# Optimization experiments

Hardware: AMD Instinct MI355X
Metric: run time of the kernel (lower is better)

Reference implementation:

```python
import jax, jax.numpy as jnp
import numpy as np

NUM_USER = 100000
NUM_ENTITY = 1000000
NUM_RELATION = 60
DIM = 32
N_NEIGHBOR = 16
N_ITER = 2
BATCH = 8192


def setup_inputs() -> dict:
    key = jax.random.key(0)
    ks = jax.random.split(key, 9)
    users = jax.random.randint(ks[0], (BATCH,), 0, NUM_USER)
    items = jax.random.randint(ks[1], (BATCH,), 0, NUM_ENTITY)
    entity_emb = jax.random.normal(ks[2], (NUM_ENTITY, DIM), dtype=jnp.float32) * 0.1
    relation_emb = jax.random.normal(ks[3], (NUM_RELATION, DIM), dtype=jnp.float32) * 0.1
    adj_entity = jax.random.randint(ks[4], (NUM_ENTITY, N_NEIGHBOR), 0, NUM_ENTITY)
    adj_relation = jax.random.randint(ks[5], (NUM_ENTITY, N_NEIGHBOR), 0, NUM_RELATION)
    user_history = jax.random.randint(ks[6], (NUM_USER, N_NEIGHBOR), 0, NUM_ENTITY)
    W = jax.random.normal(ks[7], (DIM, DIM), dtype=jnp.float32) / np.sqrt(DIM)
    b = jnp.zeros((DIM,), dtype=jnp.float32)
    return {"users": users, "items": items, "entity_emb": entity_emb,
            "relation_emb": relation_emb, "adj_entity": adj_entity,
            "adj_relation": adj_relation, "user_history": user_history,
            "W": W, "b": b}


def reference(users, items, entity_emb, relation_emb, adj_entity, adj_relation, user_history, W, b):
    B = users.shape[0]
    d = entity_emb.shape[1]
    K = adj_entity.shape[1]

    # user embedding: mean-pool over gathered history item embeddings
    hist = user_history[users]                         # [B, K]
    user_emb = entity_emb[hist].mean(axis=1)           # [B, d]

    # multi-hop neighbor expansion (irregular gathers)
    entities = [items.reshape(B, 1)]
    relations = []
    for h in range(N_ITER):
        e = adj_entity[entities[h]].reshape(B, -1)     # [B, K^(h+1)]
        r = adj_relation[entities[h]].reshape(B, -1)
        entities.append(e)
        relations.append(r)

    ent_vecs = [entity_emb[e] for e in entities]       # hop h: [B, K^h, d]
    rel_vecs = [relation_emb[r] for r in relations]

    def aggregate(self_v, neigh_v, neigh_r, act):
        # self_v: [B, n, d]; neigh_v/neigh_r: [B, n, K, d]
        scores = jnp.einsum('bd,bnkd->bnk', user_emb, neigh_r)
        attn = jax.nn.softmax(scores, axis=-1)          # softmax over K neighbors
        agg = jnp.einsum('bnk,bnkd->bnd', attn, neigh_v)
        return act((self_v + agg) @ W + b)

    for it in range(N_ITER):
        act = jnp.tanh if it == N_ITER - 1 else jax.nn.sigmoid
        ent_vecs = [
            aggregate(ent_vecs[h],
                      ent_vecs[h + 1].reshape(B, -1, K, d),
                      rel_vecs[h].reshape(B, -1, K, d),
                      act)
            for h in range(N_ITER - it)
        ]

    item_emb = ent_vecs[0].reshape(B, d)
    scores = jnp.sum(user_emb * item_emb, axis=1)
    return jax.nn.sigmoid(scores)
```

## Files before the change

kernel.cpp:

```cpp
#include <hip/hip_runtime.h>


#define NT 256

__device__ __forceinline__ float sigmoidf_(float x) { return 1.0f / (1.0f + __expf(-x)); }

__global__ __launch_bounds__(NT) void mkgcn_wpe(
    const int* __restrict__ users,
    const int* __restrict__ items,
    const float* __restrict__ E,
    const float* __restrict__ R,
    const int* __restrict__ adjE,
    const int* __restrict__ adjR,
    const int* __restrict__ uhist,
    const float* __restrict__ Wg,
    const float* __restrict__ bg,
    float* __restrict__ out,
    int B)
{
    struct PE {
        int   e2[256];
        float attn[256];
        float v1[16][32];
        float x1[16][32];
        float ue[32];
        float sdot[64];
        float attn0[16];
        float v0[32];
        float x0[32];
        float h0[32];
    };
    __shared__ __align__(16) float Wl[32][32];
    __shared__ float bl[32];
    __shared__ __align__(16) PE pe[4];

    const int t = threadIdx.x;
    const int w = t >> 6;
    const int L = t & 63;
    int b = blockIdx.x * 4 + w;
    if (b >= B) b = B - 1;
    PE& P = pe[w];

    const int user = users[b];
    const int item = items[b];

    int hid = 0, e1v = 0, r1v = 0;
    if (L < 16)       hid = uhist[(long)user * 16 + L];
    else if (L < 32)  e1v = adjE[(long)item * 16 + (L - 16)];
    else if (L < 48)  r1v = adjR[(long)item * 16 + (L - 32)];
    else if (L < 56)  ((float4*)P.v0)[L - 48] = ((const float4*)(E + (long)item * 32))[L - 48];
    ((float4*)Wl)[t] = ((const float4*)Wg)[t];
    if (t < 32) bl[t] = bg[t];

    const int v  = L & 7;
    const int r8 = L >> 3;

    {
        const int h0i = __shfl(hid, r8);
        const int h1i = __shfl(hid, r8 + 8);
        const float4 a = ((const float4*)(E + (long)h0i * 32))[v];
        const float4 c = ((const float4*)(E + (long)h1i * 32))[v];
        float sx = a.x + c.x, sy = a.y + c.y, sz = a.z + c.z, sw = a.w + c.w;
        #pragma unroll
        for (int off = 8; off < 64; off <<= 1) {
            sx += __shfl_xor(sx, off); sy += __shfl_xor(sy, off);
            sz += __shfl_xor(sz, off); sw += __shfl_xor(sw, off);
        }
        if (L < 8) {
            float4 u; u.x = sx * 0.0625f; u.y = sy * 0.0625f;
            u.z = sz * 0.0625f; u.w = sw * 0.0625f;
            ((float4*)P.ue)[L] = u;
        }
    }
    {
        const int n = L >> 2, c4 = L & 3;
        const int e1n = __shfl(e1v, 16 + n);
        const int4 ev = ((const int4*)(adjE + (long)e1n * 16))[c4];
        const int4 rv = ((const int4*)(adjR + (long)e1n * 16))[c4];
        int* x1i = (int*)P.x1;
        P.e2[(c4 * 4 + 0) * 16 + n] = ev.x;  P.e2[(c4 * 4 + 1) * 16 + n] = ev.y;
        P.e2[(c4 * 4 + 2) * 16 + n] = ev.z;  P.e2[(c4 * 4 + 3) * 16 + n] = ev.w;
        x1i[(c4 * 4 + 0) * 16 + n] = rv.x;   x1i[(c4 * 4 + 1) * 16 + n] = rv.y;
        x1i[(c4 * 4 + 2) * 16 + n] = rv.z;   x1i[(c4 * 4 + 3) * 16 + n] = rv.w;
    }
    #pragma unroll
    for (int it = 0; it < 2; ++it) {
        const int r = r8 + 8 * it;
        const int e1r = __shfl(e1v, 16 + r);
        ((float4*)P.v1)[r * 8 + v] = ((const float4*)(E + (long)e1r * 32))[v];
    }
    __syncthreads();

    if (L < 60) {
        const float4* rr = (const float4*)(R + L * 32);
        const float4* uu = (const float4*)P.ue;
        float s = 0.f;
        #pragma unroll
        for (int j = 0; j < 8; ++j) {
            const float4 a = rr[j], u = uu[j];
            s += a.x * u.x + a.y * u.y + a.z * u.z + a.w * u.w;
        }
        P.sdot[L] = s;
    }
    __syncthreads();

    {
        const int* r2T = (const int*)P.x1;
        #pragma unroll
        for (int c = 0; c < 4; ++c) {
            const int k = L & 15, n = c * 4 + (L >> 4);
            const float s = P.sdot[r2T[k * 16 + n]];
            float m = s;
            #pragma unroll
            for (int off = 1; off < 16; off <<= 1) m = fmaxf(m, __shfl_xor(m, off, 16));
            const float e = __expf(s - m);
            float sum = e;
            #pragma unroll
            for (int off = 1; off < 16; off <<= 1) sum += __shfl_xor(sum, off, 16);
            P.attn[k * 16 + n] = e / sum;
        }
    }
    const int r1L = __shfl(r1v, 32 + (L & 15));
    if (L < 16) {
        const float s = P.sdot[r1L];
        float m = s;
        #pragma unroll
        for (int off = 1; off < 16; off <<= 1) m = fmaxf(m, __shfl_xor(m, off, 16));
        const float e = __expf(s - m);
        float sum = e;
        #pragma unroll
        for (int off = 1; off < 16; off <<= 1) sum += __shfl_xor(sum, off, 16);
        P.attn0[L] = e / sum;
    }
    __syncthreads();

    {
        const int n  = L >> 2;
        const int s0 = (L & 3) * 2;
        float ax0 = 0, ay0 = 0, az0 = 0, aw0 = 0;
        float ax1 = 0, ay1 = 0, az1 = 0, aw1 = 0;
        #pragma unroll 4
        for (int k = 0; k < 16; ++k) {
            const int   row = P.e2[k * 16 + n];
            const float aw  = P.attn[k * 16 + n];
            const float4* er = (const float4*)(E + (long)row * 32);
            const float4 f0 = er[s0];
            const float4 f1 = er[s0 + 1];
            ax0 += aw * f0.x; ay0 += aw * f0.y; az0 += aw * f0.z; aw0 += aw * f0.w;
            ax1 += aw * f1.x; ay1 += aw * f1.y; az1 += aw * f1.z; aw1 += aw * f1.w;
        }
        const float4 va = ((const float4*)P.v1)[n * 8 + s0];
        const float4 vb = ((const float4*)P.v1)[n * 8 + s0 + 1];
        float4 xa, xb;
        xa.x = va.x + ax0; xa.y = va.y + ay0; xa.z = va.z + az0; xa.w = va.w + aw0;
        xb.x = vb.x + ax1; xb.y = vb.y + ay1; xb.z = vb.z + az1; xb.w = vb.w + aw1;
        ((float4*)P.x1)[n * 8 + s0]     = xa;
        ((float4*)P.x1)[n * 8 + s0 + 1] = xb;
    }
    __syncthreads();

    const int dp = L & 31, half = L >> 5;
    {
        float hv[8];
        #pragma unroll
        for (int p = 0; p < 8; ++p) {
            const int n = p * 2 + half;
            float acc = bl[dp];
            #pragma unroll
            for (int d = 0; d < 32; ++d) acc += P.x1[n][d] * Wl[d][dp];
            hv[p] = sigmoidf_(acc);
        }
        #pragma unroll
        for (int p = 0; p < 8; ++p) P.x1[p * 2 + half][dp] = hv[p];
    }
    if (L < 32) {
        float a = 0.f;
        #pragma unroll
        for (int k = 0; k < 16; ++k) a += P.attn0[k] * P.v1[k][L];
        P.x0[L] = P.v0[L] + a;
    }
    __syncthreads();

    if (L < 32) {
        float acc = bl[L];
        #pragma unroll
        for (int d = 0; d < 32; ++d) acc += P.x0[d] * Wl[d][L];
        P.h0[L] = sigmoidf_(acc);
    }
    __syncthreads();

    if (L < 32) {
        float a = 0.f;
        #pragma unroll
        for (int k = 0; k < 16; ++k) a += P.attn0[k] * P.x1[k][L];
        P.x0[L] = P.h0[L] + a;
    }
    __syncthreads();

    if (L < 32) {
        float acc = bl[L];
        #pragma unroll
        for (int d = 0; d < 32; ++d) acc += P.x0[d] * Wl[d][L];
        const float ie = tanhf(acc);
        float pr = P.ue[L] * ie;
        #pragma unroll
        for (int off = 1; off < 32; off <<= 1) pr += __shfl_xor(pr, off, 32);
        if (L == 0) out[b] = sigmoidf_(pr);
    }
}

extern "C" void kernel_launch(void* const* d_in, const int* in_sizes, int n_in,
                              void* d_out, int out_size, void* d_ws, size_t ws_size,
                              hipStream_t stream) {
    const int* users   = (const int*)d_in[0];
    const int* items   = (const int*)d_in[1];
    const float* E     = (const float*)d_in[2];
    const float* R     = (const float*)d_in[3];
    const int* adjE    = (const int*)d_in[4];
    const int* adjR    = (const int*)d_in[5];
    const int* uhist   = (const int*)d_in[6];
    const float* Wg    = (const float*)d_in[7];
    const float* bg    = (const float*)d_in[8];
    float* out         = (float*)d_out;

    const int B = in_sizes[0];
    const int grid = (B + 3) / 4;
    mkgcn_wpe<<<grid, NT, 0, stream>>>(users, items, E, R, adjE, adjR, uhist, Wg, bg, out, B);
}
```

Baseline: 283.4 us.

## Replace block barriers with wave-local fences and shrink per-wave shared memory

Each wavefront handles one batch element in its own shared-memory slice, so most block-wide __syncthreads are replaced by compiler memory fences, leaving one barrier before the W use. The x1, v0, h0 and bias arrays are removed, with buffers reused (relation indices in attn, x1 in v1) and values kept in registers. This cuts LDS use so more blocks fit per CU (launch bounds hint 7), vectorises the W matvecs with float4 reads, and unrolls the gather loop further. It depends on wave-synchronous LDS visibility without real barriers, which is fragile.

After: 283.1 us. About the same (-0.1%).

```diff
diff --git a/kernel.cpp b/kernel.cpp
--- a/kernel.cpp
+++ b/kernel.cpp
@@ -2,10 +2,11 @@
 
 
 #define NT 256
+#define WFENCE() asm volatile("" ::: "memory")
 
 __device__ __forceinline__ float sigmoidf_(float x) { return 1.0f / (1.0f + __expf(-x)); }
 
-__global__ __launch_bounds__(NT) void mkgcn_wpe(
+__global__ __launch_bounds__(NT, 7) void mkgcn_wpe(
     const int* __restrict__ users,
     const int* __restrict__ items,
     const float* __restrict__ E,
@@ -22,16 +23,12 @@
         int   e2[256];
         float attn[256];
         float v1[16][32];
-        float x1[16][32];
         float ue[32];
         float sdot[64];
         float attn0[16];
-        float v0[32];
         float x0[32];
-        float h0[32];
     };
     __shared__ __align__(16) float Wl[32][32];
-    __shared__ float bl[32];
     __shared__ __align__(16) PE pe[4];
 
     const int t = threadIdx.x;
@@ -45,12 +42,13 @@
     const int item = items[b];
 
     int hid = 0, e1v = 0, r1v = 0;
+    float v0r = 0.f;
     if (L < 16)       hid = uhist[(long)user * 16 + L];
     else if (L < 32)  e1v = adjE[(long)item * 16 + (L - 16)];
     else if (L < 48)  r1v = adjR[(long)item * 16 + (L - 32)];
-    else if (L < 56)  ((float4*)P.v0)[L - 48] = ((const float4*)(E + (long)item * 32))[L - 48];
+    if (L < 32)       v0r = E[(long)item * 32 + L];
     ((float4*)Wl)[t] = ((const float4*)Wg)[t];
-    if (t < 32) bl[t] = bg[t];
+    const float bv = bg[L & 31];
 
     const int v  = L & 7;
     const int r8 = L >> 3;
@@ -77,11 +75,11 @@
         const int e1n = __shfl(e1v, 16 + n);
         const int4 ev = ((const int4*)(adjE + (long)e1n * 16))[c4];
         const int4 rv = ((const int4*)(adjR + (long)e1n * 16))[c4];
-        int* x1i = (int*)P.x1;
+        int* r2Ti = (int*)P.attn;
         P.e2[(c4 * 4 + 0) * 16 + n] = ev.x;  P.e2[(c4 * 4 + 1) * 16 + n] = ev.y;
         P.e2[(c4 * 4 + 2) * 16 + n] = ev.z;  P.e2[(c4 * 4 + 3) * 16 + n] = ev.w;
-        x1i[(c4 * 4 + 0) * 16 + n] = rv.x;   x1i[(c4 * 4 + 1) * 16 + n] = rv.y;
-        x1i[(c4 * 4 + 2) * 16 + n] = rv.z;   x1i[(c4 * 4 + 3) * 16 + n] = rv.w;
+        r2Ti[(c4 * 4 + 0) * 16 + n] = rv.x;  r2Ti[(c4 * 4 + 1) * 16 + n] = rv.y;
+        r2Ti[(c4 * 4 + 2) * 16 + n] = rv.z;  r2Ti[(c4 * 4 + 3) * 16 + n] = rv.w;
     }
     #pragma unroll
     for (int it = 0; it < 2; ++it) {
@@ -89,7 +87,7 @@
         const int e1r = __shfl(e1v, 16 + r);
         ((float4*)P.v1)[r * 8 + v] = ((const float4*)(E + (long)e1r * 32))[v];
     }
-    __syncthreads();
+    WFENCE();
 
     if (L < 60) {
         const float4* rr = (const float4*)(R + L * 32);
@@ -102,10 +100,10 @@
         }
         P.sdot[L] = s;
     }
-    __syncthreads();
-
-    {
-        const int* r2T = (const int*)P.x1;
+    WFENCE();
+
+    {
+        const int* r2T = (const int*)P.attn;
         #pragma unroll
         for (int c = 0; c < 4; ++c) {
             const int k = L & 15, n = c * 4 + (L >> 4);
@@ -132,14 +130,22 @@
         for (int off = 1; off < 16; off <<= 1) sum += __shfl_xor(sum, off, 16);
         P.attn0[L] = e / sum;
     }
-    __syncthreads();
+    WFENCE();
+
+    if (L < 32) {
+        float a = 0.f;
+        #pragma unroll
+        for (int k = 0; k < 16; ++k) a += P.attn0[k] * P.v1[k][L];
+        P.x0[L] = v0r + a;
+    }
+    WFENCE();
 
     {
         const int n  = L >> 2;
         const int s0 = (L & 3) * 2;
         float ax0 = 0, ay0 = 0, az0 = 0, aw0 = 0;
         float ax1 = 0, ay1 = 0, az1 = 0, aw1 = 0;
-        #pragma unroll 4
+        #pragma unroll 8
         for (int k = 0; k < 16; ++k) {
             const int   row = P.e2[k * 16 + n];
             const float aw  = P.attn[k * 16 + n];
@@ -154,9 +160,10 @@
         float4 xa, xb;
         xa.x = va.x + ax0; xa.y = va.y + ay0; xa.z = va.z + az0; xa.w = va.w + aw0;
         xb.x = vb.x + ax1; xb.y = vb.y + ay1; xb.z = vb.z + az1; xb.w = vb.w + aw1;
-        ((float4*)P.x1)[n * 8 + s0]     = xa;
-        ((float4*)P.x1)[n * 8 + s0 + 1] = xb;
-    }
+        ((float4*)P.v1)[n * 8 + s0]     = xa;
+        ((float4*)P.v1)[n * 8 + s0 + 1] = xb;
+    }
+
     __syncthreads();
 
     const int dp = L & 31, half = L >> 5;
@@ -165,42 +172,59 @@
         #pragma unroll
         for (int p = 0; p < 8; ++p) {
             const int n = p * 2 + half;
-            float acc = bl[dp];
+            float acc = bv;
+            const float4* xr = (const float4*)P.v1[n];
             #pragma unroll
-            for (int d = 0; d < 32; ++d) acc += P.x1[n][d] * Wl[d][dp];
+            for (int d4 = 0; d4 < 8; ++d4) {
+                const float4 xv = xr[d4];
+                acc += xv.x * Wl[d4 * 4 + 0][dp];
+                acc += xv.y * Wl[d4 * 4 + 1][dp];
+                acc += xv.z * Wl[d4 * 4 + 2][dp];
+                acc += xv.w * Wl[d4 * 4 + 3][dp];
+            }
             hv[p] = sigmoidf_(acc);
         }
-        #pragma unroll
-        for (int p = 0; p < 8; ++p) P.x1[p * 2 + half][dp] = hv[p];
-    }
+        WFENCE();
+        #pragma unroll
+        for (int p = 0; p < 8; ++p) P.v1[p * 2 + half][dp] = hv[p];
+    }
+    WFENCE();
+
+    float h0r = 0.f;
+    if (L < 32) {
+        float acc = bv;
+        const float4* xr = (const float4*)P.x0;
+        #pragma unroll
+        for (int d4 = 0; d4 < 8; ++d4) {
+            const float4 xv = xr[d4];
+            acc += xv.x * Wl[d4 * 4 + 0][L];
+            acc += xv.y * Wl[d4 * 4 + 1][L];
+            acc += xv.z * Wl[d4 * 4 + 2][L];
+            acc += xv.w * Wl[d4 * 4 + 3][L];
+        }
+        h0r = sigmoidf_(acc);
+    }
+    WFENCE();
+
     if (L < 32) {
         float a = 0.f;
         #pragma unroll
         for (int k = 0; k < 16; ++k) a += P.attn0[k] * P.v1[k][L];
-        P.x0[L] = P.v0[L] + a;
-    }
-    __syncthreads();
-
-    if (L < 32) {
-        float acc = bl[L];
-        #pragma unroll
-        for (int d = 0; d < 32; ++d) acc += P.x0[d] * Wl[d][L];
-        P.h0[L] = sigmoidf_(acc);
-    }
-    __syncthreads();
-
-    if (L < 32) {
-        float a = 0.f;
-        #pragma unroll
-        for (int k = 0; k < 16; ++k) a += P.attn0[k] * P.x1[k][L];
-        P.x0[L] = P.h0[L] + a;
-    }
-    __syncthreads();
-
-    if (L < 32) {
-        float acc = bl[L];
-        #pragma unroll
-        for (int d = 0; d < 32; ++d) acc += P.x0[d] * Wl[d][L];
+        P.x0[L] = h0r + a;
+    }
+    WFENCE();
+
+    if (L < 32) {
+        float acc = bv;
+        const float4* xr = (const float4*)P.x0;
+        #pragma unroll
+        for (int d4 = 0; d4 < 8; ++d4) {
+            const float4 xv = xr[d4];
+            acc += xv.x * Wl[d4 * 4 + 0][L];
+            acc += xv.y * Wl[d4 * 4 + 1][L];
+            acc += xv.z * Wl[d4 * 4 + 2][L];
+            acc += xv.w * Wl[d4 * 4 + 3][L];
+        }
         const float ie = tanhf(acc);
         float pr = P.ue[L] * ie;
         #pragma unroll
```
